# Optimization experiments

Measured on AMD Instinct MI355X. Metric: run time of the kernel, lower is better.

Reference implementation:

```python
import jax, jax.numpy as jnp
import numpy as np

N_NODES = 400      # total nodes across batch
B = 10             # graphs in batch (40 nodes each)
N_CONFIGS = 1000   # fixed by tile dataset
CONFIG_FEAT_DIM = 24
NODE_FEAT_DIM = 85  # continuous cols; node_feat has +1 col for shape-ele-type idx
N_SHAPE_TYPES = 8
SHAPE_EMB = 4
N_OPS = 120
OP_EMB = 32
H = 64             # h_dim
E = 800            # edges
CAT_DIM = NODE_FEAT_DIM + SHAPE_EMB + OP_EMB + CONFIG_FEAT_DIM  # 145


def _lin(k, i, o):
    return jax.random.normal(k, (i, o), jnp.float32) * (1.0 / np.sqrt(i))


def setup_inputs() -> dict:
    key = jax.random.key(0)
    ks = jax.random.split(key, 32)
    node_cont = jax.random.normal(ks[0], (N_NODES, NODE_FEAT_DIM), jnp.float32)
    shape_type = jax.random.randint(ks[1], (N_NODES, 1), 0, N_SHAPE_TYPES).astype(jnp.float32)
    node_feat = jnp.concatenate([node_cont, shape_type], axis=-1)  # [N, 86]
    node_opcode = jax.random.randint(ks[2], (N_NODES,), 0, N_OPS)
    config_feat = jax.random.normal(ks[3], (B * N_CONFIGS, CONFIG_FEAT_DIM), jnp.float32)
    edge_index = jax.random.randint(ks[4], (2, E), 0, N_NODES)
    batch = jnp.arange(N_NODES) // (N_NODES // B)  # 40 nodes per graph
    inp = dict(
        node_feat=node_feat, node_opcode=node_opcode, config_feat=config_feat,
        edge_index=edge_index, batch=batch,
        op_emb=jax.random.normal(ks[5], (N_OPS, OP_EMB), jnp.float32),
        shape_emb=jax.random.normal(ks[6], (N_SHAPE_TYPES, SHAPE_EMB), jnp.float32),
        W1=_lin(ks[7], CAT_DIM, 2 * H), b1=jnp.zeros((2 * H,), jnp.float32),
        W2=_lin(ks[8], 2 * H, 2 * H), b2=jnp.zeros((2 * H,), jnp.float32),
        Wl0=_lin(ks[9], 2 * H, H), Wr0=_lin(ks[10], 2 * H, H), bg0=jnp.zeros((H,), jnp.float32),
        Wl1=_lin(ks[11], H, H), Wr1=_lin(ks[12], H, H), bg1=jnp.zeros((H,), jnp.float32),
        Wl2=_lin(ks[13], H, H), Wr2=_lin(ks[14], H, H), bg2=jnp.zeros((H,), jnp.float32),
        Wp1=_lin(ks[15], H, H // 2), bp1=jnp.zeros((H // 2,), jnp.float32),
        Wp2=_lin(ks[16], H // 2, 1), bp2=jnp.zeros((1,), jnp.float32),
    )
    return inp


def _sage(x, src, dst, Wl, Wr, b, n):
    # PyG SAGEConv: lin_l(x) + lin_r(mean_{j->i} x_j), applied over [N, C, D]
    agg = jax.ops.segment_sum(x[src], dst, num_segments=n)
    deg = jax.ops.segment_sum(jnp.ones((src.shape[0],), x.dtype), dst, num_segments=n)
    mean = agg / jnp.maximum(deg, 1.0)[:, None, None]
    return x @ Wl + mean @ Wr + b


def reference(node_feat, node_opcode, config_feat, edge_index, batch,
              op_emb, shape_emb, W1, b1, W2, b2,
              Wl0, Wr0, bg0, Wl1, Wr1, bg1, Wl2, Wr2, bg2,
              Wp1, bp1, Wp2, bp2):
    n = node_feat.shape[0]
    cfg = config_feat.reshape(-1, N_CONFIGS, CONFIG_FEAT_DIM)  # [B, 1000, 24]
    ste = shape_emb[node_feat[:, -1].astype(jnp.int32)]        # [N, 4]
    op = op_emb[node_opcode]                                   # [N, 32]
    xn = jnp.concatenate([node_feat[:, :-1], ste, op], axis=-1)  # [N, 121]
    xn = jnp.broadcast_to(xn[:, None, :], (n, N_CONFIGS, xn.shape[-1]))
    xc = cfg[batch]  # repeat_interleave(cfg, n_nodes, dim=0) -> per-node config
    x = jnp.concatenate([xn, xc], axis=-1)                     # [N, 1000, 145]
    x = jax.nn.relu(x @ W1 + b1)
    x = jax.nn.relu(x @ W2 + b2)                               # [N, 1000, 128]
    src, dst = edge_index[0], edge_index[1]
    for Wl, Wr, bg in ((Wl0, Wr0, bg0), (Wl1, Wr1, bg1), (Wl2, Wr2, bg2)):
        x = jax.nn.relu(_sage(x, src, dst, Wl, Wr, bg, n))     # [N, 1000, 64]
    xf = x.reshape(n, -1)                                      # [N, 64000]
    cnt = jax.ops.segment_sum(jnp.ones((n,), xf.dtype), batch, num_segments=B)
    xg = jax.ops.segment_max(xf, batch, num_segments=B) \
         + jax.ops.segment_sum(xf, batch, num_segments=B) / jnp.maximum(cnt, 1.0)[:, None]
    xg = xg.reshape(B, N_CONFIGS, -1)                          # [B, 1000, 64]
    xg = xg / jnp.linalg.norm(xg, axis=-1, keepdims=True)
    out = (jax.nn.relu(xg @ Wp1 + bp1) @ Wp2 + bp2)[..., 0]    # [B, 1000]
    return out
```

## Files before the change

### kernel.cpp

```cpp
#include <hip/hip_runtime.h>
#include <hip/hip_bf16.h>

typedef unsigned short u16;
typedef short bf16x8 __attribute__((ext_vector_type(8)));
typedef float f32x4 __attribute__((ext_vector_type(4)));

#define NN 400
#define NB 10
#define NC 1000
#define CFD 24
#define NFD 85
#define NFROW 86
#define SEDIM 4
#define OEDIM 32
#define XND 121
#define EE 800
#define N_SHAPE_GUARD 7

__device__ __forceinline__ float b2f(u16 u) { return __uint_as_float((unsigned)u << 16); }
__device__ __forceinline__ u16 f2b(float v) {
  unsigned x = __float_as_uint(v);
  return (u16)((x + 0x7fff + ((x >> 16) & 1)) >> 16);
}
__device__ __forceinline__ unsigned f2b2(float lo, float hi) {
  unsigned r;
  asm("v_cvt_pk_bf16_f32 %0, %1, %2" : "=v"(r) : "v"(lo), "v"(hi));
  return r;
}
__device__ __forceinline__ float ldf(const void* p, int idx, int fz) {
  if (fz) return ((const float*)p)[idx];
  return b2f(((const u16*)p)[idx]);
}
__device__ __forceinline__ void stf(void* p, int idx, int fz, float v) {
  if (fz) { ((float*)p)[idx] = v; return; }
  ((u16*)p)[idx] = f2b(v);
}

__device__ __forceinline__ void detect_wave0(const void* W1, int t, int* flagl) {
  if (t < 64) {
    int wild = 0;
    const u16* wv = (const u16*)W1;
    for (int j = t; j < 512; j += 64) {
      float a = fabsf(b2f(wv[j]));
      if (!(a < 1e4f)) wild++;
    }
    #pragma unroll
    for (int off = 32; off; off >>= 1) wild += __shfl_xor(wild, off);
    if (t == 0) *flagl = (wild > 16) ? 1 : 0;
  }
}

__global__ __launch_bounds__(256) void k_prep_all(
    const void* __restrict__ node_feat, const int* __restrict__ opcode,
    const void* __restrict__ cfg, const int* __restrict__ edge_index,
    const void* __restrict__ op_emb, const void* __restrict__ shape_emb,
    const void* __restrict__ W1, const void* __restrict__ b1,
    const void* __restrict__ W2,
    const void* __restrict__ Wl0, const void* __restrict__ Wr0,
    const void* __restrict__ Wl1, const void* __restrict__ Wr1,
    const void* __restrict__ Wl2, const void* __restrict__ Wr2,
    float* __restrict__ A_node, float* __restrict__ C_cfg,
    u16* __restrict__ W2t, u16* __restrict__ Wc0t,
    u16* __restrict__ Wc1t, u16* __restrict__ Wc2t,
    int* __restrict__ offs, int* __restrict__ srcl,
    int* __restrict__ perm) {
  __shared__ int flagl;
  int t = threadIdx.x;
  detect_wave0(W1, t, &flagl);
  __syncthreads();
  int fz = flagl;
  int bid = blockIdx.x;

  if (bid < 313) {
    __shared__ float w1l[CFD * 128];
    __shared__ float cfl[32 * CFD];
    int r0 = bid * 32;
    for (int idx = t; idx < CFD * 128; idx += 256)
      w1l[idx] = ldf(W1, (XND + (idx >> 7)) * 128 + (idx & 127), fz);
    for (int idx = t; idx < 32 * CFD; idx += 256) {
      int r = idx / CFD, k = idx - r * CFD;
      if (r0 + r < 10000) cfl[idx] = ldf(cfg, (r0 + r) * CFD + k, fz);
    }
    __syncthreads();
    int rg = t >> 5;
    int cg = t & 31;
    float acc[4][4] = {};
    for (int k = 0; k < CFD; k++) {
      float4 bb = *reinterpret_cast<const float4*>(&w1l[k * 128 + cg * 4]);
      #pragma unroll
      for (int ri = 0; ri < 4; ri++) {
        float a = cfl[(rg * 4 + ri) * CFD + k];
        acc[ri][0] += a * bb.x;
        acc[ri][1] += a * bb.y;
        acc[ri][2] += a * bb.z;
        acc[ri][3] += a * bb.w;
      }
    }
    #pragma unroll
    for (int ri = 0; ri < 4; ri++) {
      int row = r0 + rg * 4 + ri;
      if (row < 10000) {
        float4 o;
        o.x = acc[ri][0]; o.y = acc[ri][1]; o.z = acc[ri][2]; o.w = acc[ri][3];
        *reinterpret_cast<float4*>(&C_cfg[(size_t)row * 128 + cg * 4]) = o;
      }
    }
    return;
  }
  if (bid < 363) {
    __shared__ float w1m[XND * 128];
    __shared__ float xnl[8 * 128];
    int i0 = (bid - 313) * 8;
    for (int idx = t; idx < XND * 128; idx += 256) w1m[idx] = ldf(W1, idx, fz);
    for (int idx = t; idx < 1024; idx += 256) {
      int node = idx >> 7, tt = idx & 127;
      int i = i0 + node;
      float v = 0.f;
      if (tt < NFD) {
        v = ldf(node_feat, i * NFROW + tt, fz);
      } else if (tt < NFD + SEDIM) {
        int st = (int)ldf(node_feat, i * NFROW + NFD, fz);
        st = min(max(st, 0), N_SHAPE_GUARD);
        v = ldf(shape_emb, st * SEDIM + (tt - NFD), fz);
      } else if (tt < XND) {
        int oc = min(max(opcode[i], 0), 119);
        v = ldf(op_emb, oc * OEDIM + (tt - NFD - SEDIM), fz);
      }
      xnl[idx] = v;
    }
    __syncthreads();
    int ng = t >> 6;
    int c2 = (t & 63) * 2;
    float a00 = ldf(b1, c2, fz), a01 = ldf(b1, c2 + 1, fz);
    float a10 = a00, a11 = a01;
    for (int k = 0; k < XND; k++) {
      float2 wv = *reinterpret_cast<const float2*>(&w1m[k * 128 + c2]);
      float x0 = xnl[(ng * 2) * 128 + k];
      float x1 = xnl[(ng * 2 + 1) * 128 + k];
      a00 += x0 * wv.x; a01 += x0 * wv.y;
      a10 += x1 * wv.x; a11 += x1 * wv.y;
    }
    int i = i0 + ng * 2;
    float2 s0; s0.x = a00; s0.y = a01;
    float2 s1; s1.x = a10; s1.y = a11;
    *reinterpret_cast<float2*>(&A_node[i * 128 + c2]) = s0;
    *reinterpret_cast<float2*>(&A_node[(i + 1) * 128 + c2]) = s1;
    return;
  }
  if (bid < 555) {
    int idx = (bid - 363) * 256 + t;
    if (idx < 16384) {
      int n = idx >> 7, k = idx & 127;
      W2t[idx] = f2b(ldf(W2, k * 128 + n, fz)); return;
    }
    idx -= 16384;
    if (idx < 16384) {
      int n = idx >> 7, k = idx & 127;
      float v = (n < 64) ? ldf(Wl0, k * 64 + n, fz) : ldf(Wr0, k * 64 + n - 64, fz);
      Wc0t[idx] = f2b(v); return;
    }
    idx -= 16384;
    if (idx < 8192) {
      int n = idx >> 6, k = idx & 63;
      float v = (n < 64) ? ldf(Wl1, k * 64 + n, fz) : ldf(Wr1, k * 64 + n - 64, fz);
      Wc1t[idx] = f2b(v); return;
    }
    idx -= 8192;
    if (idx < 8192) {
      int n = idx >> 6, k = idx & 63;
      float v = (n < 64) ? ldf(Wl2, k * 64 + n, fz) : ldf(Wr2, k * 64 + n - 64, fz);
      Wc2t[idx] = f2b(v); return;
    }
    return;
  }
  {
    __shared__ int cnt[NN];
    __shared__ int offl[NN + 1];
    __shared__ int dbin[64];
    for (int i = t; i < NN; i += 256) cnt[i] = 0;
    __syncthreads();
    for (int e = t; e < EE; e += 256) {
      int d = edge_index[EE + e] & 511; if (d < NN) atomicAdd(&cnt[d], 1);
    }
    __syncthreads();
    if (t == 0) {
      int s = 0;
      for (int i = 0; i < NN; i++) { offl[i] = s; s += cnt[i]; }
      offl[NN] = s;
    }
    __syncthreads();
    for (int i = t; i < NN; i += 256) cnt[i] = offl[i];
    for (int i = t; i < NN + 1; i += 256) offs[i] = offl[i];
    __syncthreads();
    for (int e = t; e < EE; e += 256) {
      int d = edge_index[EE + e] & 511;
      if (d < NN) {
        int p = atomicAdd(&cnt[d], 1);
        srcl[p] = min(max(edge_index[e], 0), NN - 1);
      }
    }
    for (int i = t; i < 64; i += 256) dbin[i] = 0;
    __syncthreads();
    for (int i = t; i < NN; i += 256) {
      int d = min(offl[i + 1] - offl[i], 63);
      atomicAdd(&dbin[d], 1);
    }
    __syncthreads();
    if (t == 0) {
      int s = 0;
      for (int d = 0; d < 64; d++) { int c = dbin[d]; dbin[d] = s; s += c; }
    }
    __syncthreads();
    for (int i = t; i < NN; i += 256) {
      int d = min(offl[i + 1] - offl[i], 63);
      int p = atomicAdd(&dbin[d], 1);
      perm[p] = i;
    }
  }
}

__global__ __launch_bounds__(512, 1) void k_fused(
    const float* __restrict__ A_node, const float* __restrict__ C_cfg,
    const int* __restrict__ batch, const int* __restrict__ offs,
    const int* __restrict__ srcl, const int* __restrict__ perm,
    const u16* __restrict__ W2t, const u16* __restrict__ Wc0t,
    const u16* __restrict__ Wc1t, const u16* __restrict__ Wc2t,
    const void* __restrict__ b2, const void* __restrict__ bg0,
    const void* __restrict__ bg1, const void* __restrict__ bg2,
    const void* __restrict__ Wp1, const void* __restrict__ bp1,
    const void* __restrict__ Wp2, const void* __restrict__ bp2,
    const void* __restrict__ W1d, void* __restrict__ out) {
  __shared__ __align__(16) u16 xbuf[401 * 128];
  __shared__ __align__(16) u16 ybuf[401 * 64];
  __shared__ int offsl[NN + 1];
  __shared__ int srcll[EE];
  __shared__ int perml[NN];
  __shared__ int flagl;

  int c = blockIdx.x;
  int t = threadIdx.x;
  int w = t >> 6, l = t & 63;
  int lm = l & 15, quad = l >> 4;

  detect_wave0(W1d, t, &flagl);
  float* cfgl = (float*)ybuf;
  for (int idx = t; idx < 1280; idx += 512)
    cfgl[idx] = C_cfg[((size_t)(idx >> 7) * NC + c) * 128 + (idx & 127)];
  for (int idx = t; idx < NN + 1; idx += 512) offsl[idx] = offs[idx];
  for (int idx = t; idx < EE; idx += 512) srcll[idx] = srcl[idx];
  for (int idx = t; idx < NN; idx += 512) perml[idx] = perm[idx];
  for (int idx = t; idx < 128; idx += 512) xbuf[NN * 128 + idx] = 0;
  if (t < 64) ybuf[NN * 64 + t] = 0;
  __syncthreads();
  int fz = flagl;

  {
    float bv[8][4];
    #pragma unroll
    for (int mt = 0; mt < 8; mt++)
      #pragma unroll
      for (int rg = 0; rg < 4; rg++) bv[mt][rg] = ldf(b2, mt*16 + quad*4 + rg, fz);

    for (int tile = w; tile < 25; tile += 8) {
      int i = tile*16 + lm;
      int b = batch[i] % NB;
      const float* an = A_node + i*128;
      const float* cf = cfgl + b*128;
      f32x4 acc[8] = {};
      #pragma unroll
      for (int kt = 0; kt < 4; kt++) {
        int ko = kt*32 + quad*8;
        float4 a0 = *(const float4*)(an + ko);
        float4 a1 = *(const float4*)(an + ko + 4);
        float4 c0 = *(const float4*)(cf + ko);
        float4 c1 = *(const float4*)(cf + ko + 4);
        union { bf16x8 v; unsigned u[4]; } f;
        f.u[0] = f2b2(fmaxf(a0.x + c0.x, 0.f), fmaxf(a0.y + c0.y, 0.f));
        f.u[1] = f2b2(fmaxf(a0.z + c0.z, 0.f), fmaxf(a0.w + c0.w, 0.f));
        f.u[2] = f2b2(fmaxf(a1.x + c1.x, 0.f), fmaxf(a1.y + c1.y, 0.f));
        f.u[3] = f2b2(fmaxf(a1.z + c1.z, 0.f), fmaxf(a1.w + c1.w, 0.f));
        bf16x8 bfr = f.v;
        bf16x8 wfk[8];
        #pragma unroll
        for (int mt = 0; mt < 8; mt++)
          wfk[mt] = *reinterpret_cast<const bf16x8*>(W2t + (mt*16 + lm)*128 + kt*32 + quad*8);
        #pragma unroll
        for (int mt = 0; mt < 8; mt++)
          acc[mt] = __builtin_amdgcn_mfma_f32_16x16x32_bf16(wfk[mt], bfr, acc[mt], 0, 0, 0);
      }
      #pragma unroll
      for (int mt = 0; mt < 8; mt++) {
        float v0 = fmaxf(acc[mt][0] + bv[mt][0], 0.f);
        float v1 = fmaxf(acc[mt][1] + bv[mt][1], 0.f);
        float v2 = fmaxf(acc[mt][2] + bv[mt][2], 0.f);
        float v3 = fmaxf(acc[mt][3] + bv[mt][3], 0.f);
        int ch = mt*2 + (quad >> 1);
        int chs = ch ^ (i & 7);
        uint2 u; u.x = f2b2(v0, v1); u.y = f2b2(v2, v3);
        *reinterpret_cast<uint2*>(&xbuf[i*128 + chs*8 + (quad & 1)*4]) = u;
      }
    }
  }
  __syncthreads();

  {
    bf16x8 wr[4][4];
    #pragma unroll
    for (int mt = 0; mt < 4; mt++)
      #pragma unroll
      for (int kt = 0; kt < 4; kt++)
        wr[mt][kt] = *reinterpret_cast<const bf16x8*>(Wc0t + (64 + mt*16 + lm)*128 + kt*32 + quad*8);
    float bv[4][4];
    #pragma unroll
    for (int mt = 0; mt < 4; mt++)
      #pragma unroll
      for (int rg = 0; rg < 4; rg++) bv[mt][rg] = ldf(bg0, mt*16 + quad*4 + rg, fz);

    for (int tile = w; tile < 25; tile += 8) {
      int i = perml[tile*16 + lm];
      int o0 = offsl[i], o1 = offsl[i + 1];
      int deg = o1 - o0;
      float rd = 1.f / fmaxf((float)deg, 1.f);
      int md = deg;
      md = max(md, __shfl_xor(md, 1));
      md = max(md, __shfl_xor(md, 2));
      md = max(md, __shfl_xor(md, 4));
      md = max(md, __shfl_xor(md, 8));
      bf16x8 xf[4];
      #pragma unroll
      for (int kt = 0; kt < 4; kt++)
        xf[kt] = *reinterpret_cast<const bf16x8*>(&xbuf[i*128 + ((kt*4 + quad) ^ (i & 7))*8]);
      f32x4 accS[4] = {}, accM[4] = {};
      #pragma unroll
      for (int kt = 0; kt < 4; kt++) {
        bf16x8 wlk[4];
        #pragma unroll
        for (int mt = 0; mt < 4; mt++)
          wlk[mt] = *reinterpret_cast<const bf16x8*>(Wc0t + (mt*16 + lm)*128 + kt*32 + quad*8);
        #pragma unroll
        for (int mt = 0; mt < 4; mt++)
          accS[mt] = __builtin_amdgcn_mfma_f32_16x16x32_bf16(wlk[mt], xf[kt], accS[mt], 0, 0, 0);
      }
      for (int r = 0; r < md; r++) {
        int sn = (r < deg) ? srcll[o0 + r] : NN;
        bf16x8 z[4];
        #pragma unroll
        for (int kt = 0; kt < 4; kt++)
          z[kt] = *reinterpret_cast<const bf16x8*>(&xbuf[sn*128 + ((kt*4 + quad) ^ (sn & 7))*8]);
        #pragma unroll
        for (int kt = 0; kt < 4; kt++)
          #pragma unroll
          for (int mt = 0; mt < 4; mt++)
            accM[mt] = __builtin_amdgcn_mfma_f32_16x16x32_bf16(wr[mt][kt], z[kt], accM[mt], 0, 0, 0);
      }
      #pragma unroll
      for (int mt = 0; mt < 4; mt++) {
        float v0 = fmaxf(accS[mt][0] + rd*accM[mt][0] + bv[mt][0], 0.f);
        float v1 = fmaxf(accS[mt][1] + rd*accM[mt][1] + bv[mt][1], 0.f);
        float v2 = fmaxf(accS[mt][2] + rd*accM[mt][2] + bv[mt][2], 0.f);
        float v3 = fmaxf(accS[mt][3] + rd*accM[mt][3] + bv[mt][3], 0.f);
        int ch = mt*2 + (quad >> 1);
        int chs = ch ^ (i & 7);
        uint2 u; u.x = f2b2(v0, v1); u.y = f2b2(v2, v3);
        *reinterpret_cast<uint2*>(&ybuf[i*64 + chs*8 + (quad & 1)*4]) = u;
      }
    }
  }
  __syncthreads();

  u16* src_buf = ybuf;
  u16* dst_buf = xbuf;
  for (int layer = 0; layer < 2; layer++) {
    const u16* Wt = (layer == 0) ? Wc1t : Wc2t;
    const void* bg = (layer == 0) ? bg1 : bg2;
    bf16x8 wr[4][2];
    #pragma unroll
    for (int mt = 0; mt < 4; mt++)
      #pragma unroll
      for (int kt = 0; kt < 2; kt++)
        wr[mt][kt] = *reinterpret_cast<const bf16x8*>(Wt + (64 + mt*16 + lm)*64 + kt*32 + quad*8);
    float bv[4][4];
    #pragma unroll
    for (int mt = 0; mt < 4; mt++)
      #pragma unroll
      for (int rg = 0; rg < 4; rg++) bv[mt][rg] = ldf(bg, mt*16 + quad*4 + rg, fz);

    for (int tile = w; tile < 25; tile += 8) {
      int i = perml[tile*16 + lm];
      int o0 = offsl[i], o1 = offsl[i + 1];
      int deg = o1 - o0;
      float rd = 1.f / fmaxf((float)deg, 1.f);
      int md = deg;
      md = max(md, __shfl_xor(md, 1));
      md = max(md, __shfl_xor(md, 2));
      md = max(md, __shfl_xor(md, 4));
      md = max(md, __shfl_xor(md, 8));
      bf16x8 xf[2];
      #pragma unroll
      for (int kt = 0; kt < 2; kt++)
        xf[kt] = *reinterpret_cast<const bf16x8*>(&src_buf[i*64 + ((kt*4 + quad) ^ (i & 7))*8]);
      f32x4 accS[4] = {}, accM[4] = {};
      #pragma unroll
      for (int kt = 0; kt < 2; kt++) {
        bf16x8 wlk[4];
        #pragma unroll
        for (int mt = 0; mt < 4; mt++)
          wlk[mt] = *reinterpret_cast<const bf16x8*>(Wt + (mt*16 + lm)*64 + kt*32 + quad*8);
        #pragma unroll
        for (int mt = 0; mt < 4; mt++)
          accS[mt] = __builtin_amdgcn_mfma_f32_16x16x32_bf16(wlk[mt], xf[kt], accS[mt], 0, 0, 0);
      }
      for (int r = 0; r < md; r++) {
        int sn = (r < deg) ? srcll[o0 + r] : NN;
        bf16x8 z[2];
        #pragma unroll
        for (int kt = 0; kt < 2; kt++)
          z[kt] = *reinterpret_cast<const bf16x8*>(&src_buf[sn*64 + ((kt*4 + quad) ^ (sn & 7))*8]);
        #pragma unroll
        for (int kt = 0; kt < 2; kt++)
          #pragma unroll
          for (int mt = 0; mt < 4; mt++)
            accM[mt] = __builtin_amdgcn_mfma_f32_16x16x32_bf16(wr[mt][kt], z[kt], accM[mt], 0, 0, 0);
      }
      #pragma unroll
      for (int mt = 0; mt < 4; mt++) {
        float v0 = fmaxf(accS[mt][0] + rd*accM[mt][0] + bv[mt][0], 0.f);
        float v1 = fmaxf(accS[mt][1] + rd*accM[mt][1] + bv[mt][1], 0.f);
        float v2 = fmaxf(accS[mt][2] + rd*accM[mt][2] + bv[mt][2], 0.f);
        float v3 = fmaxf(accS[mt][3] + rd*accM[mt][3] + bv[mt][3], 0.f);
        int ch = mt*2 + (quad >> 1);
        int chs = ch ^ (i & 7);
        uint2 u; u.x = f2b2(v0, v1); u.y = f2b2(v2, v3);
        *reinterpret_cast<uint2*>(&dst_buf[i*64 + chs*8 + (quad & 1)*4]) = u;
      }
    }
    if (t < 64) dst_buf[NN*64 + t] = 0;
    __syncthreads();
    u16* tmp = src_buf; src_buf = dst_buf; dst_buf = tmp;
  }

  {
    float* scr  = (float*)xbuf;
    float* wp1s = (float*)&xbuf[4096];
    for (int idx = t; idx < 2048; idx += 512) wp1s[idx] = ldf(Wp1, idx, fz);
    __syncthreads();
    for (int b = w; b < NB; b += 8) {
      int h = l;
      float mx = -3.0e38f, sm = 0.f;
      for (int j = 0; j < 40; j++) {
        int row = b*40 + j;
        int chs = (h >> 3) ^ (row & 7);
        float v = b2f(src_buf[row*64 + chs*8 + (h & 7)]);
        mx = fmaxf(mx, v); sm += v;
      }
      float g = mx + sm * (1.f / 40.f);
      float sq = g * g;
      #pragma unroll
      for (int off = 32; off; off >>= 1) sq += __shfl_xor(sq, off);
      float gn = g * rsqrtf(sq);
      scr[w*64 + h] = gn;
      int j32 = l & 31;
      float hj = ldf(bp1, j32, fz);
      for (int k = 0; k < 64; k++) hj += scr[w*64 + k] * wp1s[k*32 + j32];
      hj = fmaxf(hj, 0.f);
      float contrib = hj * ldf(Wp2, j32, fz);
      #pragma unroll
      for (int off = 32; off; off >>= 1) contrib += __shfl_xor(contrib, off);
      if (l == 0) stf(out, b*NC + c, fz, contrib * 0.5f + ldf(bp2, 0, fz));
    }
  }
}

extern "C" void kernel_launch(void* const* d_in, const int* in_sizes, int n_in,
                              void* d_out, int out_size, void* d_ws, size_t ws_size,
                              hipStream_t stream) {
  const void* node_feat   = d_in[0];
  const int*  node_opcode = (const int*)d_in[1];
  const void* config_feat = d_in[2];
  const int*  edge_index  = (const int*)d_in[3];
  const int*  batch       = (const int*)d_in[4];
  const void* op_emb      = d_in[5];
  const void* shape_emb   = d_in[6];
  const void* W1  = d_in[7];
  const void* b1  = d_in[8];
  const void* W2  = d_in[9];
  const void* b2  = d_in[10];
  const void* Wl0 = d_in[11];
  const void* Wr0 = d_in[12];
  const void* bg0 = d_in[13];
  const void* Wl1 = d_in[14];
  const void* Wr1 = d_in[15];
  const void* bg1 = d_in[16];
  const void* Wl2 = d_in[17];
  const void* Wr2 = d_in[18];
  const void* bg2 = d_in[19];
  const void* Wp1 = d_in[20];
  const void* bp1 = d_in[21];
  const void* Wp2 = d_in[22];
  const void* bp2 = d_in[23];

  char* p = (char*)d_ws;
  float* A_node = (float*)p; p += 400*128*4;
  float* C_cfg  = (float*)p; p += 10000*128*4;
  u16*   W2t    = (u16*)p;   p += 128*128*2;
  u16*   Wc0t   = (u16*)p;   p += 128*128*2;
  u16*   Wc1t   = (u16*)p;   p += 128*64*2;
  u16*   Wc2t   = (u16*)p;   p += 128*64*2;
  int*   offs   = (int*)p;   p += 2048;
  int*   srcl   = (int*)p;   p += 4096;
  int*   perm   = (int*)p;   p += 2048;

  k_prep_all<<<dim3(556), dim3(256), 0, stream>>>(
      node_feat, node_opcode, config_feat, edge_index, op_emb, shape_emb,
      W1, b1, W2, Wl0, Wr0, Wl1, Wr1, Wl2, Wr2,
      A_node, C_cfg, W2t, Wc0t, Wc1t, Wc2t, offs, srcl, perm);

  k_fused<<<dim3(1000), dim3(512), 0, stream>>>(
      A_node, C_cfg, batch, offs, srcl, perm, W2t, Wc0t, Wc1t, Wc2t,
      b2, bg0, bg1, bg2, Wp1, bp1, Wp2, bp2, W1, d_out);
}
```

Measured before the change: 367.8 us.

## Split first SAGE layer by K halves to shrink LDS and raise occupancy

The fused per-config kernel now computes the 128-wide MLP output in two 64-channel halves. Each half is staged in a single 64-wide LDS buffer and immediately consumed by layer-0 SAGE, so the 128-wide and 64-wide node buffers are replaced by one 400x64 buffer. Neighbor aggregation becomes a VALU mean over bf16 rows followed by one MFMA per weight, instead of an MFMA per neighbor, and later layers keep their outputs in registers across a barrier so the same buffer can be reused in place. Launch bounds go from 1 to 4 blocks per CU, and the prep kernel's serial prefix sums become wave-level shuffle scans. This trades recomputed MLP loads, extra barriers and higher register pressure (acc0 and yReg arrays) for much lower LDS per block and more blocks resident per CU.

```diff
diff --git a/kernel.cpp b/kernel.cpp
--- a/kernel.cpp
+++ b/kernel.cpp
@@ -183,10 +183,24 @@
       int d = edge_index[EE + e] & 511; if (d < NN) atomicAdd(&cnt[d], 1);
     }
     __syncthreads();
-    if (t == 0) {
-      int s = 0;
-      for (int i = 0; i < NN; i++) { offl[i] = s; s += cnt[i]; }
-      offl[NN] = s;
+    if (t < 64) {
+      int base = t * 7;
+      int lsum = 0;
+      #pragma unroll
+      for (int k = 0; k < 7; k++) { int n = base + k; if (n < NN) lsum += cnt[n]; }
+      int inc = lsum;
+      #pragma unroll
+      for (int off = 1; off < 64; off <<= 1) {
+        int v = __shfl_up(inc, off);
+        if (t >= off) inc += v;
+      }
+      int run = inc - lsum;
+      #pragma unroll
+      for (int k = 0; k < 7; k++) {
+        int n = base + k;
+        if (n < NN) { offl[n] = run; run += cnt[n]; }
+      }
+      if (t == 63) offl[NN] = run;
     }
     __syncthreads();
     for (int i = t; i < NN; i += 256) cnt[i] = offl[i];
@@ -206,9 +220,15 @@
       atomicAdd(&dbin[d], 1);
     }
     __syncthreads();
-    if (t == 0) {
-      int s = 0;
-      for (int d = 0; d < 64; d++) { int c = dbin[d]; dbin[d] = s; s += c; }
+    if (t < 64) {
+      int v = dbin[t];
+      int inc = v;
+      #pragma unroll
+      for (int off = 1; off < 64; off <<= 1) {
+        int s = __shfl_up(inc, off);
+        if (t >= off) inc += s;
+      }
+      dbin[t] = inc - v;
     }
     __syncthreads();
     for (int i = t; i < NN; i += 256) {
@@ -219,7 +239,7 @@
   }
 }
 
-__global__ __launch_bounds__(512, 1) void k_fused(
+__global__ __launch_bounds__(512, 4) void k_fused(
     const float* __restrict__ A_node, const float* __restrict__ C_cfg,
     const int* __restrict__ batch, const int* __restrict__ offs,
     const int* __restrict__ srcl, const int* __restrict__ perm,
@@ -230,227 +250,272 @@
     const void* __restrict__ Wp1, const void* __restrict__ bp1,
     const void* __restrict__ Wp2, const void* __restrict__ bp2,
     const void* __restrict__ W1d, void* __restrict__ out) {
-  __shared__ __align__(16) u16 xbuf[401 * 128];
-  __shared__ __align__(16) u16 ybuf[401 * 64];
+  __shared__ __align__(16) u16 pbuf[NN * 64];
+  __shared__ float cfgl[1280];
   __shared__ int offsl[NN + 1];
   __shared__ int srcll[EE];
   __shared__ int perml[NN];
+  __shared__ float p5w[2048];
+  __shared__ float p5s[512];
   __shared__ int flagl;
 
   int c = blockIdx.x;
   int t = threadIdx.x;
   int w = t >> 6, l = t & 63;
   int lm = l & 15, quad = l >> 4;
+  int qh = quad >> 1, ql = quad & 1;
 
   detect_wave0(W1d, t, &flagl);
-  float* cfgl = (float*)ybuf;
   for (int idx = t; idx < 1280; idx += 512)
     cfgl[idx] = C_cfg[((size_t)(idx >> 7) * NC + c) * 128 + (idx & 127)];
   for (int idx = t; idx < NN + 1; idx += 512) offsl[idx] = offs[idx];
   for (int idx = t; idx < EE; idx += 512) srcll[idx] = srcl[idx];
   for (int idx = t; idx < NN; idx += 512) perml[idx] = perm[idx];
-  for (int idx = t; idx < 128; idx += 512) xbuf[NN * 128 + idx] = 0;
-  if (t < 64) ybuf[NN * 64 + t] = 0;
   __syncthreads();
   int fz = flagl;
 
-  {
-    float bv[8][4];
+  int ni[4];
+  #pragma unroll
+  for (int tt = 0; tt < 4; tt++) {
+    int tile = w + tt * 8;
+    ni[tt] = (tile < 25) ? perml[tile * 16 + lm] : 0;
+  }
+
+  f32x4 acc0[4][4] = {};
+  for (int h = 0; h < 2; h++) {
     #pragma unroll
-    for (int mt = 0; mt < 8; mt++)
-      #pragma unroll
-      for (int rg = 0; rg < 4; rg++) bv[mt][rg] = ldf(b2, mt*16 + quad*4 + rg, fz);
-
-    for (int tile = w; tile < 25; tile += 8) {
-      int i = tile*16 + lm;
-      int b = batch[i] % NB;
-      const float* an = A_node + i*128;
-      const float* cf = cfgl + b*128;
-      f32x4 acc[8] = {};
-      #pragma unroll
-      for (int kt = 0; kt < 4; kt++) {
-        int ko = kt*32 + quad*8;
-        float4 a0 = *(const float4*)(an + ko);
-        float4 a1 = *(const float4*)(an + ko + 4);
-        float4 c0 = *(const float4*)(cf + ko);
-        float4 c1 = *(const float4*)(cf + ko + 4);
-        union { bf16x8 v; unsigned u[4]; } f;
-        f.u[0] = f2b2(fmaxf(a0.x + c0.x, 0.f), fmaxf(a0.y + c0.y, 0.f));
-        f.u[1] = f2b2(fmaxf(a0.z + c0.z, 0.f), fmaxf(a0.w + c0.w, 0.f));
-        f.u[2] = f2b2(fmaxf(a1.x + c1.x, 0.f), fmaxf(a1.y + c1.y, 0.f));
-        f.u[3] = f2b2(fmaxf(a1.z + c1.z, 0.f), fmaxf(a1.w + c1.w, 0.f));
-        bf16x8 bfr = f.v;
-        bf16x8 wfk[8];
-        #pragma unroll
-        for (int mt = 0; mt < 8; mt++)
-          wfk[mt] = *reinterpret_cast<const bf16x8*>(W2t + (mt*16 + lm)*128 + kt*32 + quad*8);
-        #pragma unroll
-        for (int mt = 0; mt < 8; mt++)
-          acc[mt] = __builtin_amdgcn_mfma_f32_16x16x32_bf16(wfk[mt], bfr, acc[mt], 0, 0, 0);
-      }
-      #pragma unroll
-      for (int mt = 0; mt < 8; mt++) {
-        float v0 = fmaxf(acc[mt][0] + bv[mt][0], 0.f);
-        float v1 = fmaxf(acc[mt][1] + bv[mt][1], 0.f);
-        float v2 = fmaxf(acc[mt][2] + bv[mt][2], 0.f);
-        float v3 = fmaxf(acc[mt][3] + bv[mt][3], 0.f);
-        int ch = mt*2 + (quad >> 1);
-        int chs = ch ^ (i & 7);
+    for (int tt = 0; tt < 4; tt++) {
+      int tile = w + tt * 8;
+      if (tile < 25) {
+        int i = ni[tt];
+        int b = batch[i] % NB;
+        const float* an = A_node + (size_t)i * 128;
+        const float* cf = cfgl + b * 128;
+        f32x4 a8[4] = {};
+        #pragma unroll
+        for (int kt = 0; kt < 4; kt++) {
+          int ko = kt * 32 + quad * 8;
+          float4 a0 = *(const float4*)(an + ko);
+          float4 a1 = *(const float4*)(an + ko + 4);
+          float4 c0 = *(const float4*)(cf + ko);
+          float4 c1 = *(const float4*)(cf + ko + 4);
+          union { bf16x8 v; unsigned u[4]; } f;
+          f.u[0] = f2b2(fmaxf(a0.x + c0.x, 0.f), fmaxf(a0.y + c0.y, 0.f));
+          f.u[1] = f2b2(fmaxf(a0.z + c0.z, 0.f), fmaxf(a0.w + c0.w, 0.f));
+          f.u[2] = f2b2(fmaxf(a1.x + c1.x, 0.f), fmaxf(a1.y + c1.y, 0.f));
+          f.u[3] = f2b2(fmaxf(a1.z + c1.z, 0.f), fmaxf(a1.w + c1.w, 0.f));
+          bf16x8 bfr = f.v;
+          #pragma unroll
+          for (int mt = 0; mt < 4; mt++) {
+            bf16x8 w2f = *reinterpret_cast<const bf16x8*>(
+                W2t + (h * 64 + mt * 16 + lm) * 128 + kt * 32 + quad * 8);
+            a8[mt] = __builtin_amdgcn_mfma_f32_16x16x32_bf16(w2f, bfr, a8[mt], 0, 0, 0);
+          }
+        }
+        #pragma unroll
+        for (int mt = 0; mt < 4; mt++) {
+          int cb = h * 64 + mt * 16 + quad * 4;
+          float v0 = fmaxf(a8[mt][0] + ldf(b2, cb + 0, fz), 0.f);
+          float v1 = fmaxf(a8[mt][1] + ldf(b2, cb + 1, fz), 0.f);
+          float v2 = fmaxf(a8[mt][2] + ldf(b2, cb + 2, fz), 0.f);
+          float v3 = fmaxf(a8[mt][3] + ldf(b2, cb + 3, fz), 0.f);
+          uint2 u; u.x = f2b2(v0, v1); u.y = f2b2(v2, v3);
+          int gs = (mt * 2 + qh) ^ (i & 7);
+          *reinterpret_cast<uint2*>(&pbuf[i * 64 + gs * 8 + ql * 4]) = u;
+        }
+      }
+    }
+    __syncthreads();
+
+    #pragma unroll
+    for (int tt = 0; tt < 4; tt++) {
+      int tile = w + tt * 8;
+      if (tile < 25) {
+        int i = ni[tt];
+        int o0 = offsl[i], o1 = offsl[i + 1];
+        float rd = 1.f / fmaxf((float)(o1 - o0), 1.f);
+        bf16x8 xf[2];
+        #pragma unroll
+        for (int ktp = 0; ktp < 2; ktp++)
+          xf[ktp] = *reinterpret_cast<const bf16x8*>(
+              &pbuf[i * 64 + ((ktp * 4 + quad) ^ (i & 7)) * 8]);
+        float s8[2][8] = {};
+        int e = o0;
+        for (; e + 1 < o1; e += 2) {
+          int sn0 = srcll[e], sn1 = srcll[e + 1];
+          bf16x8 z0[2], z1[2];
+          #pragma unroll
+          for (int ktp = 0; ktp < 2; ktp++) {
+            z0[ktp] = *reinterpret_cast<const bf16x8*>(
+                &pbuf[sn0 * 64 + ((ktp * 4 + quad) ^ (sn0 & 7)) * 8]);
+            z1[ktp] = *reinterpret_cast<const bf16x8*>(
+                &pbuf[sn1 * 64 + ((ktp * 4 + quad) ^ (sn1 & 7)) * 8]);
+          }
+          #pragma unroll
+          for (int ktp = 0; ktp < 2; ktp++)
+            #pragma unroll
+            for (int j = 0; j < 8; j++) {
+              s8[ktp][j] += b2f((u16)z0[ktp][j]);
+              s8[ktp][j] += b2f((u16)z1[ktp][j]);
+            }
+        }
+        if (e < o1) {
+          int sn0 = srcll[e];
+          #pragma unroll
+          for (int ktp = 0; ktp < 2; ktp++) {
+            bf16x8 zv = *reinterpret_cast<const bf16x8*>(
+                &pbuf[sn0 * 64 + ((ktp * 4 + quad) ^ (sn0 & 7)) * 8]);
+            #pragma unroll
+            for (int j = 0; j < 8; j++) s8[ktp][j] += b2f((u16)zv[j]);
+          }
+        }
+        #pragma unroll
+        for (int ktp = 0; ktp < 2; ktp++) {
+          union { bf16x8 v; unsigned u[4]; } f;
+          f.u[0] = f2b2(s8[ktp][0] * rd, s8[ktp][1] * rd);
+          f.u[1] = f2b2(s8[ktp][2] * rd, s8[ktp][3] * rd);
+          f.u[2] = f2b2(s8[ktp][4] * rd, s8[ktp][5] * rd);
+          f.u[3] = f2b2(s8[ktp][6] * rd, s8[ktp][7] * rd);
+          bf16x8 mf = f.v;
+          int kt = h * 2 + ktp;
+          #pragma unroll
+          for (int mt = 0; mt < 4; mt++) {
+            bf16x8 wlf = *reinterpret_cast<const bf16x8*>(
+                Wc0t + (mt * 16 + lm) * 128 + kt * 32 + quad * 8);
+            bf16x8 wrf = *reinterpret_cast<const bf16x8*>(
+                Wc0t + (64 + mt * 16 + lm) * 128 + kt * 32 + quad * 8);
+            acc0[tt][mt] = __builtin_amdgcn_mfma_f32_16x16x32_bf16(wlf, xf[ktp], acc0[tt][mt], 0, 0, 0);
+            acc0[tt][mt] = __builtin_amdgcn_mfma_f32_16x16x32_bf16(wrf, mf, acc0[tt][mt], 0, 0, 0);
+          }
+        }
+      }
+    }
+    __syncthreads();
+  }
+
+  #pragma unroll
+  for (int tt = 0; tt < 4; tt++) {
+    int tile = w + tt * 8;
+    if (tile < 25) {
+      int i = ni[tt];
+      #pragma unroll
+      for (int mt = 0; mt < 4; mt++) {
+        int cb = mt * 16 + quad * 4;
+        float v0 = fmaxf(acc0[tt][mt][0] + ldf(bg0, cb + 0, fz), 0.f);
+        float v1 = fmaxf(acc0[tt][mt][1] + ldf(bg0, cb + 1, fz), 0.f);
+        float v2 = fmaxf(acc0[tt][mt][2] + ldf(bg0, cb + 2, fz), 0.f);
+        float v3 = fmaxf(acc0[tt][mt][3] + ldf(bg0, cb + 3, fz), 0.f);
         uint2 u; u.x = f2b2(v0, v1); u.y = f2b2(v2, v3);
-        *reinterpret_cast<uint2*>(&xbuf[i*128 + chs*8 + (quad & 1)*4]) = u;
+        int gs = (mt * 2 + qh) ^ (i & 7);
+        *reinterpret_cast<uint2*>(&pbuf[i * 64 + gs * 8 + ql * 4]) = u;
       }
     }
   }
   __syncthreads();
 
-  {
-    bf16x8 wr[4][4];
-    #pragma unroll
-    for (int mt = 0; mt < 4; mt++)
-      #pragma unroll
-      for (int kt = 0; kt < 4; kt++)
-        wr[mt][kt] = *reinterpret_cast<const bf16x8*>(Wc0t + (64 + mt*16 + lm)*128 + kt*32 + quad*8);
-    float bv[4][4];
-    #pragma unroll
-    for (int mt = 0; mt < 4; mt++)
-      #pragma unroll
-      for (int rg = 0; rg < 4; rg++) bv[mt][rg] = ldf(bg0, mt*16 + quad*4 + rg, fz);
-
-    for (int tile = w; tile < 25; tile += 8) {
-      int i = perml[tile*16 + lm];
-      int o0 = offsl[i], o1 = offsl[i + 1];
-      int deg = o1 - o0;
-      float rd = 1.f / fmaxf((float)deg, 1.f);
-      int md = deg;
-      md = max(md, __shfl_xor(md, 1));
-      md = max(md, __shfl_xor(md, 2));
-      md = max(md, __shfl_xor(md, 4));
-      md = max(md, __shfl_xor(md, 8));
-      bf16x8 xf[4];
-      #pragma unroll
-      for (int kt = 0; kt < 4; kt++)
-        xf[kt] = *reinterpret_cast<const bf16x8*>(&xbuf[i*128 + ((kt*4 + quad) ^ (i & 7))*8]);
-      f32x4 accS[4] = {}, accM[4] = {};
-      #pragma unroll
-      for (int kt = 0; kt < 4; kt++) {
-        bf16x8 wlk[4];
-        #pragma unroll
-        for (int mt = 0; mt < 4; mt++)
-          wlk[mt] = *reinterpret_cast<const bf16x8*>(Wc0t + (mt*16 + lm)*128 + kt*32 + quad*8);
-        #pragma unroll
-        for (int mt = 0; mt < 4; mt++)
-          accS[mt] = __builtin_amdgcn_mfma_f32_16x16x32_bf16(wlk[mt], xf[kt], accS[mt], 0, 0, 0);
-      }
-      for (int r = 0; r < md; r++) {
-        int sn = (r < deg) ? srcll[o0 + r] : NN;
-        bf16x8 z[4];
-        #pragma unroll
-        for (int kt = 0; kt < 4; kt++)
-          z[kt] = *reinterpret_cast<const bf16x8*>(&xbuf[sn*128 + ((kt*4 + quad) ^ (sn & 7))*8]);
-        #pragma unroll
-        for (int kt = 0; kt < 4; kt++)
-          #pragma unroll
-          for (int mt = 0; mt < 4; mt++)
-            accM[mt] = __builtin_amdgcn_mfma_f32_16x16x32_bf16(wr[mt][kt], z[kt], accM[mt], 0, 0, 0);
-      }
-      #pragma unroll
-      for (int mt = 0; mt < 4; mt++) {
-        float v0 = fmaxf(accS[mt][0] + rd*accM[mt][0] + bv[mt][0], 0.f);
-        float v1 = fmaxf(accS[mt][1] + rd*accM[mt][1] + bv[mt][1], 0.f);
-        float v2 = fmaxf(accS[mt][2] + rd*accM[mt][2] + bv[mt][2], 0.f);
-        float v3 = fmaxf(accS[mt][3] + rd*accM[mt][3] + bv[mt][3], 0.f);
-        int ch = mt*2 + (quad >> 1);
-        int chs = ch ^ (i & 7);
-        uint2 u; u.x = f2b2(v0, v1); u.y = f2b2(v2, v3);
-        *reinterpret_cast<uint2*>(&ybuf[i*64 + chs*8 + (quad & 1)*4]) = u;
-      }
-    }
-  }
-  __syncthreads();
-
-  u16* src_buf = ybuf;
-  u16* dst_buf = xbuf;
   for (int layer = 0; layer < 2; layer++) {
     const u16* Wt = (layer == 0) ? Wc1t : Wc2t;
     const void* bg = (layer == 0) ? bg1 : bg2;
-    bf16x8 wr[4][2];
+    uint2 yReg[4][4];
     #pragma unroll
-    for (int mt = 0; mt < 4; mt++)
-      #pragma unroll
-      for (int kt = 0; kt < 2; kt++)
-        wr[mt][kt] = *reinterpret_cast<const bf16x8*>(Wt + (64 + mt*16 + lm)*64 + kt*32 + quad*8);
-    float bv[4][4];
+    for (int tt = 0; tt < 4; tt++) {
+      int tile = w + tt * 8;
+      if (tile < 25) {
+        int i = ni[tt];
+        int o0 = offsl[i], o1 = offsl[i + 1];
+        float rd = 1.f / fmaxf((float)(o1 - o0), 1.f);
+        bf16x8 xf[2];
+        #pragma unroll
+        for (int kt = 0; kt < 2; kt++)
+          xf[kt] = *reinterpret_cast<const bf16x8*>(
+              &pbuf[i * 64 + ((kt * 4 + quad) ^ (i & 7)) * 8]);
+        float s8[2][8] = {};
+        int e = o0;
+        for (; e + 1 < o1; e += 2) {
+          int sn0 = srcll[e], sn1 = srcll[e + 1];
+          bf16x8 z0[2], z1[2];
+          #pragma unroll
+          for (int kt = 0; kt < 2; kt++) {
+            z0[kt] = *reinterpret_cast<const bf16x8*>(
+                &pbuf[sn0 * 64 + ((kt * 4 + quad) ^ (sn0 & 7)) * 8]);
+            z1[kt] = *reinterpret_cast<const bf16x8*>(
+                &pbuf[sn1 * 64 + ((kt * 4 + quad) ^ (sn1 & 7)) * 8]);
+          }
+          #pragma unroll
+          for (int kt = 0; kt < 2; kt++)
+            #pragma unroll
+            for (int j = 0; j < 8; j++) {
+              s8[kt][j] += b2f((u16)z0[kt][j]);
+              s8[kt][j] += b2f((u16)z1[kt][j]);
+            }
+        }
+        if (e < o1) {
+          int sn0 = srcll[e];
+          #pragma unroll
+          for (int kt = 0; kt < 2; kt++) {
+            bf16x8 zv = *reinterpret_cast<const bf16x8*>(
+                &pbuf[sn0 * 64 + ((kt * 4 + quad) ^ (sn0 & 7)) * 8]);
+            #pragma unroll
+            for (int j = 0; j < 8; j++) s8[kt][j] += b2f((u16)zv[j]);
+          }
+        }
+        f32x4 a2[4] = {};
+        #pragma unroll
+        for (int kt = 0; kt < 2; kt++) {
+          union { bf16x8 v; unsigned u[4]; } f;
+          f.u[0] = f2b2(s8[kt][0] * rd, s8[kt][1] * rd);
+          f.u[1] = f2b2(s8[kt][2] * rd, s8[kt][3] * rd);
+          f.u[2] = f2b2(s8[kt][4] * rd, s8[kt][5] * rd);
+          f.u[3] = f2b2(s8[kt][6] * rd, s8[kt][7] * rd);
+          bf16x8 mf = f.v;
+          #pragma unroll
+          for (int mt = 0; mt < 4; mt++) {
+            bf16x8 wlf = *reinterpret_cast<const bf16x8*>(
+                Wt + (mt * 16 + lm) * 64 + kt * 32 + quad * 8);
+            bf16x8 wrf = *reinterpret_cast<const bf16x8*>(
+                Wt + (64 + mt * 16 + lm) * 64 + kt * 32 + quad * 8);
+            a2[mt] = __builtin_amdgcn_mfma_f32_16x16x32_bf16(wlf, xf[kt], a2[mt], 0, 0, 0);
+            a2[mt] = __builtin_amdgcn_mfma_f32_16x16x32_bf16(wrf, mf, a2[mt], 0, 0, 0);
+          }
+        }
+        #pragma unroll
+        for (int mt = 0; mt < 4; mt++) {
+          int cb = mt * 16 + quad * 4;
+          float v0 = fmaxf(a2[mt][0] + ldf(bg, cb + 0, fz), 0.f);
+          float v1 = fmaxf(a2[mt][1] + ldf(bg, cb + 1, fz), 0.f);
+          float v2 = fmaxf(a2[mt][2] + ldf(bg, cb + 2, fz), 0.f);
+          float v3 = fmaxf(a2[mt][3] + ldf(bg, cb + 3, fz), 0.f);
+          yReg[tt][mt].x = f2b2(v0, v1);
+          yReg[tt][mt].y = f2b2(v2, v3);
+        }
+      }
+    }
+    __syncthreads();
     #pragma unroll
-    for (int mt = 0; mt < 4; mt++)
-      #pragma unroll
-      for (int rg = 0; rg < 4; rg++) bv[mt][rg] = ldf(bg, mt*16 + quad*4 + rg, fz);
-
-    for (int tile = w; tile < 25; tile += 8) {
-      int i = perml[tile*16 + lm];
-      int o0 = offsl[i], o1 = offsl[i + 1];
-      int deg = o1 - o0;
-      float rd = 1.f / fmaxf((float)deg, 1.f);
-      int md = deg;
-      md = max(md, __shfl_xor(md, 1));
-      md = max(md, __shfl_xor(md, 2));
-      md = max(md, __shfl_xor(md, 4));
-      md = max(md, __shfl_xor(md, 8));
-      bf16x8 xf[2];
-      #pragma unroll
-      for (int kt = 0; kt < 2; kt++)
-        xf[kt] = *reinterpret_cast<const bf16x8*>(&src_buf[i*64 + ((kt*4 + quad) ^ (i & 7))*8]);
-      f32x4 accS[4] = {}, accM[4] = {};
-      #pragma unroll
-      for (int kt = 0; kt < 2; kt++) {
-        bf16x8 wlk[4];
-        #pragma unroll
-        for (int mt = 0; mt < 4; mt++)
-          wlk[mt] = *reinterpret_cast<const bf16x8*>(Wt + (mt*16 + lm)*64 + kt*32 + quad*8);
-        #pragma unroll
-        for (int mt = 0; mt < 4; mt++)
-          accS[mt] = __builtin_amdgcn_mfma_f32_16x16x32_bf16(wlk[mt], xf[kt], accS[mt], 0, 0, 0);
-      }
-      for (int r = 0; r < md; r++) {
-        int sn = (r < deg) ? srcll[o0 + r] : NN;
-        bf16x8 z[2];
-        #pragma unroll
-        for (int kt = 0; kt < 2; kt++)
-          z[kt] = *reinterpret_cast<const bf16x8*>(&src_buf[sn*64 + ((kt*4 + quad) ^ (sn & 7))*8]);
-        #pragma unroll
-        for (int kt = 0; kt < 2; kt++)
-          #pragma unroll
-          for (int mt = 0; mt < 4; mt++)
-            accM[mt] = __builtin_amdgcn_mfma_f32_16x16x32_bf16(wr[mt][kt], z[kt], accM[mt], 0, 0, 0);
-      }
-      #pragma unroll
-      for (int mt = 0; mt < 4; mt++) {
-        float v0 = fmaxf(accS[mt][0] + rd*accM[mt][0] + bv[mt][0], 0.f);
-        float v1 = fmaxf(accS[mt][1] + rd*accM[mt][1] + bv[mt][1], 0.f);
-        float v2 = fmaxf(accS[mt][2] + rd*accM[mt][2] + bv[mt][2], 0.f);
-        float v3 = fmaxf(accS[mt][3] + rd*accM[mt][3] + bv[mt][3], 0.f);
-        int ch = mt*2 + (quad >> 1);
-        int chs = ch ^ (i & 7);
-        uint2 u; u.x = f2b2(v0, v1); u.y = f2b2(v2, v3);
-        *reinterpret_cast<uint2*>(&dst_buf[i*64 + chs*8 + (quad & 1)*4]) = u;
-      }
-    }
-    if (t < 64) dst_buf[NN*64 + t] = 0;
-    __syncthreads();
-    u16* tmp = src_buf; src_buf = dst_buf; dst_buf = tmp;
+    for (int tt = 0; tt < 4; tt++) {
+      int tile = w + tt * 8;
+      if (tile < 25) {
+        int i = ni[tt];
+        #pragma unroll
+        for (int mt = 0; mt < 4; mt++) {
+          int gs = (mt * 2 + qh) ^ (i & 7);
+          *reinterpret_cast<uint2*>(&pbuf[i * 64 + gs * 8 + ql * 4]) = yReg[tt][mt];
+        }
+      }
+    }
+    __syncthreads();
   }
 
   {
-    float* scr  = (float*)xbuf;
-    float* wp1s = (float*)&xbuf[4096];
-    for (int idx = t; idx < 2048; idx += 512) wp1s[idx] = ldf(Wp1, idx, fz);
+    for (int idx = t; idx < 2048; idx += 512) p5w[idx] = ldf(Wp1, idx, fz);
     __syncthreads();
     for (int b = w; b < NB; b += 8) {
       int h = l;
       float mx = -3.0e38f, sm = 0.f;
       for (int j = 0; j < 40; j++) {
-        int row = b*40 + j;
+        int row = b * 40 + j;
         int chs = (h >> 3) ^ (row & 7);
-        float v = b2f(src_buf[row*64 + chs*8 + (h & 7)]);
+        float v = b2f(pbuf[row * 64 + chs * 8 + (h & 7)]);
         mx = fmaxf(mx, v); sm += v;
       }
       float g = mx + sm * (1.f / 40.f);
@@ -458,15 +523,15 @@
       #pragma unroll
       for (int off = 32; off; off >>= 1) sq += __shfl_xor(sq, off);
       float gn = g * rsqrtf(sq);
-      scr[w*64 + h] = gn;
+      p5s[w * 64 + h] = gn;
       int j32 = l & 31;
       float hj = ldf(bp1, j32, fz);
-      for (int k = 0; k < 64; k++) hj += scr[w*64 + k] * wp1s[k*32 + j32];
+      for (int k = 0; k < 64; k++) hj += p5s[w * 64 + k] * p5w[k * 32 + j32];
       hj = fmaxf(hj, 0.f);
       float contrib = hj * ldf(Wp2, j32, fz);
       #pragma unroll
       for (int off = 32; off; off >>= 1) contrib += __shfl_xor(contrib, off);
-      if (l == 0) stf(out, b*NC + c, fz, contrib * 0.5f + ldf(bp2, 0, fz));
+      if (l == 0) stf(out, b * NC + c, fz, contrib * 0.5f + ldf(bp2, 0, fz));
     }
   }
 }
```

Measured after the change: 608.7 us. +65.5%, slower.
